# Kernel tuning notes

Hardware: AMD Instinct MI355X
Metric: run time of the kernel (lower is better)

Reference implementation:

```python
import jax, jax.numpy as jnp
import numpy as np

B, N, D_IN, C_OUT = 16, 512, 256, 32
CS, H, W_GRID = 48, 256, 256


def setup_inputs() -> dict:
    key = jax.random.key(0)
    k1, k2, k3, k4 = jax.random.split(key, 4)
    spatial_info = jax.random.normal(k1, (B, CS, H, W_GRID), dtype=jnp.float32)
    entity_embeddings = jax.random.normal(k2, (B, N, D_IN), dtype=jnp.float32)
    W = jax.random.normal(k3, (D_IN, C_OUT), dtype=jnp.float32) * (D_IN ** -0.5)
    b = jnp.zeros((C_OUT,), dtype=jnp.float32)
    entity_location = jax.random.randint(k4, (B, N, 2), 0, H, dtype=jnp.int64)
    return {"spatial_info": spatial_info, "entity_embeddings": entity_embeddings,
            "W": W, "b": b, "entity_location": entity_location}


def reference(spatial_info, entity_embeddings, W, b, entity_location):
    # scatter_project: fc_block == Linear
    proj = jnp.einsum('bnd,dc->bnc', entity_embeddings, W) + b  # [B, N, C]
    Bsz, Cs, Hh, Ww = spatial_info.shape
    h = entity_location[..., 0]  # [B, N]
    w = entity_location[..., 1]  # [B, N]
    b_idx = jnp.arange(Bsz)[:, None]  # [B, 1]
    # single fused parallel scatter (replaces the python double loop);
    # channels-last layout so each entity writes a contiguous C-vector
    scatter_map = jnp.zeros((Bsz, Hh, Ww, proj.shape[-1]), proj.dtype)
    scatter_map = scatter_map.at[b_idx, h, w].set(proj)
    scatter_map = jnp.transpose(scatter_map, (0, 3, 1, 2))  # [B, C, H, W]
    return jnp.concatenate([spatial_info, scatter_map], axis=1)
```

## Files before the change

kernel.cpp:

```cpp
#include <hip/hip_runtime.h>

#define BB   16
#define NN   512
#define DIN  256
#define COUT 32
#define CCS  48
#define HH   256
#define WWG  256
#define HW   (HH * WWG)
#define CTOT (CCS + COUT)

__global__ void k_init_winner(int* __restrict__ winner) {
    int i = blockIdx.x * blockDim.x + threadIdx.x;
    if (i < BB * HW) winner[i] = -1;
}

__global__ void k_winner(const int* __restrict__ loc, int* __restrict__ winner) {
    int i = blockIdx.x * blockDim.x + threadIdx.x;
    if (i >= BB * NN) return;
    int b = i / NN;
    int n = i - b * NN;
    int h = loc[2 * i + 0];
    int w = loc[2 * i + 1];
    atomicMax(&winner[b * HW + h * WWG + w], n);
}

__global__ void k_proj(const float* __restrict__ emb, const float* __restrict__ Wm,
                       const float* __restrict__ bias, float* __restrict__ proj) {
    __shared__ float Wl[DIN * COUT];
    int tid = threadIdx.x;
    for (int i = tid; i < DIN * COUT; i += blockDim.x) Wl[i] = Wm[i];
    __syncthreads();
    int c = tid & 31;
    int r = tid >> 5;
    int row = blockIdx.x * 8 + r;
    if (row >= BB * NN) return;
    const float* e = emb + (size_t)row * DIN;
    float acc = bias[c];
    #pragma unroll 8
    for (int d = 0; d < DIN; ++d)
        acc += e[d] * Wl[d * COUT + c];
    proj[(size_t)row * COUT + c] = acc;
}

__global__ void k_fill(const float* __restrict__ sp, float* __restrict__ out) {
    long long i4 = (long long)blockIdx.x * blockDim.x + threadIdx.x;
    const long long TOT4 = (long long)BB * CTOT * HW / 4;
    if (i4 >= TOT4) return;
    long long i = i4 * 4;
    int pix = (int)(i % HW);
    long long t = i / HW;
    int ch = (int)(t % CTOT);
    int b  = (int)(t / CTOT);
    float4 v;
    if (ch < CCS) {
        v = *(const float4*)(sp + ((size_t)(b * CCS + ch) * HW + pix));
    } else {
        v = make_float4(0.f, 0.f, 0.f, 0.f);
    }
    *(float4*)(out + i) = v;
}

__global__ void k_scatter(const float* __restrict__ proj, const int* __restrict__ loc,
                          const int* __restrict__ winner, float* __restrict__ out) {
    int t = blockIdx.x * blockDim.x + threadIdx.x;
    if (t >= BB * NN * COUT) return;
    int c = t & 31;
    int i = t >> 5;
    int b = i / NN;
    int n = i - b * NN;
    int h = loc[2 * i + 0];
    int w = loc[2 * i + 1];
    int cell = b * HW + h * WWG + w;
    if (winner[cell] != n) return;
    out[((size_t)b * CTOT + CCS + c) * HW + (size_t)h * WWG + w] =
        proj[(size_t)i * COUT + c];
}

extern "C" void kernel_launch(void* const* d_in, const int* in_sizes, int n_in,
                              void* d_out, int out_size, void* d_ws, size_t ws_size,
                              hipStream_t stream) {
    const float* sp   = (const float*)d_in[0];
    const float* emb  = (const float*)d_in[1];
    const float* Wm   = (const float*)d_in[2];
    const float* bias = (const float*)d_in[3];
    const int*   loc  = (const int*)d_in[4];
    float* out = (float*)d_out;

    float* proj  = (float*)d_ws;
    int* winner  = (int*)((char*)d_ws + (size_t)BB * NN * COUT * 4);

    hipLaunchKernelGGL(k_init_winner, dim3((BB * HW + 255) / 256), dim3(256), 0, stream,
                       winner);
    hipLaunchKernelGGL(k_proj, dim3(BB * NN / 8), dim3(256), 0, stream,
                       emb, Wm, bias, proj);
    hipLaunchKernelGGL(k_winner, dim3((BB * NN + 255) / 256), dim3(256), 0, stream,
                       loc, winner);
    const long long TOT4 = (long long)BB * CTOT * HW / 4;
    hipLaunchKernelGGL(k_fill, dim3((unsigned)((TOT4 + 255) / 256)), dim3(256), 0, stream,
                       sp, out);
    hipLaunchKernelGGL(k_scatter, dim3(BB * NN * COUT / 256), dim3(256), 0, stream,
                       proj, loc, winner, out);
}
```

Measured before the change: 138.1 us.

## Merge projection and winner kernels, use memset, 3D nontemporal fill grid

Merges the projection and winner-atomic kernels into one launch that splits work by block index. The winner-init kernel is replaced by hipMemsetAsync. The fill kernel now uses a 3D grid that removes 64-bit div/mod, and it uses nontemporal loads and stores for the large streaming copy. Divisions in the scatter kernel become shifts. The aim is fewer launches, cheaper index math and less cache pollution, while the main bandwidth-bound copy stays the same size.

```diff
diff --git a/kernel.cpp b/kernel.cpp
--- a/kernel.cpp
+++ b/kernel.cpp
@@ -1,4 +1,6 @@
 #include <hip/hip_runtime.h>
+
+typedef float f4 __attribute__((ext_vector_type(4)));
 
 #define BB   16
 #define NN   512
@@ -10,70 +12,61 @@
 #define HW   (HH * WWG)
 #define CTOT (CCS + COUT)
 
-__global__ void k_init_winner(int* __restrict__ winner) {
-    int i = blockIdx.x * blockDim.x + threadIdx.x;
-    if (i < BB * HW) winner[i] = -1;
+__global__ __launch_bounds__(256) void k_projwin(
+        const float* __restrict__ emb, const float* __restrict__ Wm,
+        const float* __restrict__ bias, const int* __restrict__ loc,
+        float* __restrict__ proj, int* __restrict__ winner) {
+    __shared__ float Wl[DIN * COUT];
+    int tid = threadIdx.x;
+    if (blockIdx.x < 1024) {
+        for (int i = tid; i < DIN * COUT; i += 256) Wl[i] = Wm[i];
+        __syncthreads();
+        int c = tid & 31;
+        int r = tid >> 5;
+        int row = blockIdx.x * 8 + r;
+        const float* e = emb + (size_t)row * DIN;
+        float acc = bias[c];
+        #pragma unroll 8
+        for (int d = 0; d < DIN; ++d)
+            acc += e[d] * Wl[d * COUT + c];
+        proj[(size_t)row * COUT + c] = acc;
+    } else {
+        int i = (blockIdx.x - 1024) * 256 + tid;
+        int b = i >> 9;
+        int n = i & (NN - 1);
+        int h = loc[2 * i + 0];
+        int w = loc[2 * i + 1];
+        atomicMax(&winner[b * HW + h * WWG + w], n);
+    }
 }
 
-__global__ void k_winner(const int* __restrict__ loc, int* __restrict__ winner) {
-    int i = blockIdx.x * blockDim.x + threadIdx.x;
-    if (i >= BB * NN) return;
-    int b = i / NN;
-    int n = i - b * NN;
-    int h = loc[2 * i + 0];
-    int w = loc[2 * i + 1];
-    atomicMax(&winner[b * HW + h * WWG + w], n);
+__global__ __launch_bounds__(256) void k_fill(const float* __restrict__ sp,
+                                              float* __restrict__ out) {
+    int pix4 = blockIdx.x * 256 + threadIdx.x;
+    int ch = blockIdx.y;
+    int b  = blockIdx.z;
+    f4 v = (f4)(0.0f);
+    if (ch < CCS) {
+        const f4* s = (const f4*)sp + (((size_t)(b * CCS + ch) << 14) + pix4);
+        v = __builtin_nontemporal_load(s);
+    }
+    f4* o = (f4*)out + (((size_t)(b * CTOT + ch) << 14) + pix4);
+    __builtin_nontemporal_store(v, o);
 }
 
-__global__ void k_proj(const float* __restrict__ emb, const float* __restrict__ Wm,
-                       const float* __restrict__ bias, float* __restrict__ proj) {
-    __shared__ float Wl[DIN * COUT];
-    int tid = threadIdx.x;
-    for (int i = tid; i < DIN * COUT; i += blockDim.x) Wl[i] = Wm[i];
-    __syncthreads();
-    int c = tid & 31;
-    int r = tid >> 5;
-    int row = blockIdx.x * 8 + r;
-    if (row >= BB * NN) return;
-    const float* e = emb + (size_t)row * DIN;
-    float acc = bias[c];
-    #pragma unroll 8
-    for (int d = 0; d < DIN; ++d)
-        acc += e[d] * Wl[d * COUT + c];
-    proj[(size_t)row * COUT + c] = acc;
-}
-
-__global__ void k_fill(const float* __restrict__ sp, float* __restrict__ out) {
-    long long i4 = (long long)blockIdx.x * blockDim.x + threadIdx.x;
-    const long long TOT4 = (long long)BB * CTOT * HW / 4;
-    if (i4 >= TOT4) return;
-    long long i = i4 * 4;
-    int pix = (int)(i % HW);
-    long long t = i / HW;
-    int ch = (int)(t % CTOT);
-    int b  = (int)(t / CTOT);
-    float4 v;
-    if (ch < CCS) {
-        v = *(const float4*)(sp + ((size_t)(b * CCS + ch) * HW + pix));
-    } else {
-        v = make_float4(0.f, 0.f, 0.f, 0.f);
-    }
-    *(float4*)(out + i) = v;
-}
-
-__global__ void k_scatter(const float* __restrict__ proj, const int* __restrict__ loc,
-                          const int* __restrict__ winner, float* __restrict__ out) {
-    int t = blockIdx.x * blockDim.x + threadIdx.x;
-    if (t >= BB * NN * COUT) return;
+__global__ __launch_bounds__(256) void k_scatter(
+        const float* __restrict__ proj, const int* __restrict__ loc,
+        const int* __restrict__ winner, float* __restrict__ out) {
+    int t = blockIdx.x * 256 + threadIdx.x;
     int c = t & 31;
     int i = t >> 5;
-    int b = i / NN;
-    int n = i - b * NN;
+    int b = i >> 9;
+    int n = i & (NN - 1);
     int h = loc[2 * i + 0];
     int w = loc[2 * i + 1];
     int cell = b * HW + h * WWG + w;
     if (winner[cell] != n) return;
-    out[((size_t)b * CTOT + CCS + c) * HW + (size_t)h * WWG + w] =
+    out[((size_t)(b * CTOT + CCS + c) << 16) + (size_t)h * WWG + w] =
         proj[(size_t)i * COUT + c];
 }
 
@@ -88,17 +81,16 @@
     float* out = (float*)d_out;
 
     float* proj  = (float*)d_ws;
-    int* winner  = (int*)((char*)d_ws + (size_t)BB * NN * COUT * 4);
+    int*   winner = (int*)((char*)d_ws + (size_t)BB * NN * COUT * 4);
 
-    hipLaunchKernelGGL(k_init_winner, dim3((BB * HW + 255) / 256), dim3(256), 0, stream,
-                       winner);
-    hipLaunchKernelGGL(k_proj, dim3(BB * NN / 8), dim3(256), 0, stream,
-                       emb, Wm, bias, proj);
-    hipLaunchKernelGGL(k_winner, dim3((BB * NN + 255) / 256), dim3(256), 0, stream,
-                       loc, winner);
-    const long long TOT4 = (long long)BB * CTOT * HW / 4;
-    hipLaunchKernelGGL(k_fill, dim3((unsigned)((TOT4 + 255) / 256)), dim3(256), 0, stream,
+    hipMemsetAsync(winner, 0xFF, (size_t)BB * HW * sizeof(int), stream);
+
+    hipLaunchKernelGGL(k_projwin, dim3(1024 + BB * NN / 256), dim3(256), 0, stream,
+                       emb, Wm, bias, loc, proj, winner);
+
+    hipLaunchKernelGGL(k_fill, dim3(HW / 4 / 256, CTOT, BB), dim3(256), 0, stream,
                        sp, out);
+
     hipLaunchKernelGGL(k_scatter, dim3(BB * NN * COUT / 256), dim3(256), 0, stream,
                        proj, loc, winner, out);
 }
```

Measured after the change: 116.6 us. 1.18x faster.
